# Performance work log

Hardware: AMD Instinct MI355X
Metric: run time of the kernel (lower is better)

## Reference

```python
import jax, jax.numpy as jnp
import numpy as np

C = 201      # num_classes (200 + background)
K = 5        # num_prototype
D = 256      # projected dim
GAMMA = 0.999
SK_EPS = 0.05
SK_ITERS = 3


def l2n(x, eps=1e-12):
    return x / jnp.maximum(jnp.linalg.norm(x, axis=-1, keepdims=True), eps)


def layernorm(x, g, b, eps=1e-5):
    mu = jnp.mean(x, axis=-1, keepdims=True)
    var = jnp.var(x, axis=-1, keepdims=True)
    return (x - mu) * jax.lax.rsqrt(var + eps) * g + b


def masked_sinkhorn(logits, mask_f):
    # logits: [N, K] prototype logits for one class; mask_f: [N] 1.0 where patch belongs to class
    m = mask_f[:, None]
    L = jnp.exp(logits / SK_EPS) * m
    Bc = mask_f.sum()  # number of patches of this class
    L = L / jnp.maximum(jnp.sum(L), 1e-12)
    for _ in range(SK_ITERS):
        L = L / jnp.maximum(jnp.sum(L, axis=0, keepdims=True), 1e-12) / K   # per-prototype marginal
        L = L / jnp.maximum(jnp.sum(L, axis=1, keepdims=True), 1e-12) * m   # per-patch marginal (masked)
        L = L / jnp.maximum(Bc, 1.0)
    L = L * Bc
    idx = jnp.argmax(L, axis=1)                                   # prototype index per patch
    hard = jax.nn.one_hot(idx, K, dtype=logits.dtype) * m          # deterministic hard assignment
    return hard, idx


def setup_inputs() -> dict:
    key = jax.random.key(0)
    k0, k1, k2, k3 = jax.random.split(key, 4)
    B, HW, DB = 64, 256, 768
    patch_tokens = jax.random.normal(k0, (B, HW, DB), jnp.float32)
    proj_w = jax.random.normal(k1, (D, DB), jnp.float32) * (1.0 / np.sqrt(DB))
    proj_b = jnp.zeros((D,), jnp.float32)
    ln_g = jnp.ones((D,), jnp.float32)
    ln_b = jnp.zeros((D,), jnp.float32)
    prototypes = jax.random.normal(k2, (C, K, D), jnp.float32) * 0.02
    pseudo_fg_mask = jax.random.randint(k3, (B * HW,), 0, C, dtype=jnp.int32)
    return dict(patch_tokens=patch_tokens, proj_w=proj_w, proj_b=proj_b,
                ln_g=ln_g, ln_b=ln_b, prototypes=prototypes,
                pseudo_fg_mask=pseudo_fg_mask)


def reference(patch_tokens, proj_w, proj_b, ln_g, ln_b, prototypes, pseudo_fg_mask):
    B, HW, _ = patch_tokens.shape
    H = W = int(np.sqrt(HW))
    patches = jnp.einsum('bnd,ed->bne', patch_tokens, proj_w) + proj_b      # [B,HW,D]
    patches = l2n(layernorm(patches.reshape(-1, D), ln_g, ln_b))             # [N,D] l2-normalized
    protos = l2n(prototypes)                                                 # [C,K,D] (in-place buffer normalize)
    logits_nck = jnp.einsum('nd,ckd->nck', patches, protos)                  # [N,C,K] == cosine sims
    ppl = logits_nck.reshape(B, H, W, C * K).transpose(0, 3, 1, 2)           # [B,CK,H,W]
    img_logits = jnp.mean(ppl, axis=(2, 3))                                  # AdaptiveAvgPool2d(1,1)
    pred_logits = jnp.sum(img_logits.reshape(B, C, K), axis=-1)              # == img_logits @ fc

    # ---- prototype update (vectorized over the original per-class python loop) ----
    N = patches.shape[0]
    class_preds = jnp.argmax(jnp.max(logits_nck, axis=2), axis=1)            # argmax of patch class logits
    correct_f = (pseudo_fg_mask == class_preds).astype(patches.dtype)        # [N]
    patches_correct = patches * correct_f[:, None]                           # [N,D]

    def per_class(c):
        mask_f = (pseudo_fg_mask == c).astype(patches.dtype)
        hard, idx = masked_sinkhorn(logits_nck[:, c, :], mask_f)
        L_correct = hard * correct_f[:, None]                                # [N,K]
        score = logits_nck[:, c, :] * L_correct                              # cos * assignment
        top_idx = jnp.argmax(score, axis=0)                                  # top-1 patch per prototype
        P_new_c = patches_correct[top_idx]                                   # [K,D] == final_assignment^T @ patches_correct
        return P_new_c, idx, mask_f.sum() > 0

    P_new, proto_idx, has_patches = jax.vmap(per_class)(jnp.arange(C))
    P_new = l2n(P_new)
    # final_assignment puts exactly one 1 per prototype column, so n_final != 0 always;
    # the update gate reduces to 'class has at least one patch'.
    P_upd = jnp.where(has_patches[:, None, None],
                      GAMMA * protos + (1.0 - GAMMA) * P_new, protos)
    new_prototypes = l2n(P_upd)

    per_patch_idx = jnp.take_along_axis(proto_idx.T, pseudo_fg_mask[:, None].astype(jnp.int32), axis=1)[:, 0]
    contrast_target = (per_patch_idx + K * pseudo_fg_mask).astype(patches.dtype)
    contrast_logits = logits_nck.reshape(N, C * K)
    return pred_logits, ppl, img_logits, contrast_logits, contrast_target, new_prototypes
```

## Files before the change

### kernel.cpp

```cpp
#include <hip/hip_runtime.h>
#include <hip/hip_bf16.h>

#define NROWS 16384
#define DBK   768
#define DDIM  256
#define NC    201
#define NK    5
#define NCK   1005

#define O_PPL    12864
#define O_IMG    16478784
#define O_CONTR  16543104
#define O_TGT    33009024
#define O_NEWP   33025408

#define W_PATCH  0u
#define W_PN     4194304u
#define W_CORR   4451584u
#define W_MEANP  4467968u
#define W_PBF    4484352u
#define W_PNBF   8678656u

typedef __attribute__((ext_vector_type(8))) short     short8;
typedef __attribute__((ext_vector_type(4))) float     f32x4;
typedef __attribute__((ext_vector_type(4))) unsigned int uint4v;
typedef __attribute__((ext_vector_type(4))) unsigned short ushort4v;

__device__ __forceinline__ float waveRedSum(float v){
  #pragma unroll
  for(int o=32;o>0;o>>=1) v += __shfl_xor(v,o,64);
  return v;
}

__device__ __forceinline__ unsigned short f2bf(float x){
  union { float f; unsigned u; } c; c.f = x;
  unsigned r = c.u + 0x7FFFu + ((c.u >> 16) & 1u);
  return (unsigned short)(r >> 16);
}
__device__ __forceinline__ unsigned pack2(float a, float b){
  return (unsigned)f2bf(a) | ((unsigned)f2bf(b) << 16);
}
__device__ __forceinline__ uint4v pack8(float4 lo, float4 hi){
  uint4v u;
  u[0] = pack2(lo.x, lo.y); u[1] = pack2(lo.z, lo.w);
  u[2] = pack2(hi.x, hi.y); u[3] = pack2(hi.z, hi.w);
  return u;
}

__global__ __launch_bounds__(256,2) void k_gemm1m(
    const float* __restrict__ A, const float* __restrict__ W,
    const float* __restrict__ bias, float* __restrict__ out)
{
  __shared__ ushort As[4096];
  __shared__ ushort Bs[4096];
  const int tid = threadIdx.x;
  const int m0 = blockIdx.x * 128;
  const int n0 = blockIdx.y * 128;
  const int lane = tid & 63, wid = tid >> 6;
  const int wr = wid >> 1, wc = wid & 1;
  const int srow = tid >> 2, sslot = tid & 3;
  const int woff  = srow*32      + (sslot ^ ((srow>>1)&3))*8;
  const int woff2 = (srow+64)*32 + (sslot ^ ((srow>>1)&3))*8;
  const int l15 = lane & 15, kg = lane >> 4;
  const int rslot = (kg ^ ((l15>>1)&3))*8;
  f32x4 acc[4][4] = {};
  const float* Ap0 = A + (size_t)(m0+srow)*DBK + sslot*8;
  const float* Ap1 = Ap0 + (size_t)64*DBK;
  const float* Wp0 = W + (size_t)(n0+srow)*DBK + sslot*8;
  const float* Wp1 = Wp0 + (size_t)64*DBK;
  for (int k0 = 0; k0 < DBK; k0 += 32) {
    float4 a00 = *(const float4*)(Ap0+k0), a01 = *(const float4*)(Ap0+k0+4);
    float4 a10 = *(const float4*)(Ap1+k0), a11 = *(const float4*)(Ap1+k0+4);
    float4 b00 = *(const float4*)(Wp0+k0), b01 = *(const float4*)(Wp0+k0+4);
    float4 b10 = *(const float4*)(Wp1+k0), b11 = *(const float4*)(Wp1+k0+4);
    __syncthreads();
    *(uint4v*)&As[woff]  = pack8(a00, a01);
    *(uint4v*)&As[woff2] = pack8(a10, a11);
    *(uint4v*)&Bs[woff]  = pack8(b00, b01);
    *(uint4v*)&Bs[woff2] = pack8(b10, b11);
    __syncthreads();
    short8 af[4], bf[4];
    #pragma unroll
    for (int i=0;i<4;i++){
      af[i] = *(const short8*)&As[(wr*64 + i*16 + l15)*32 + rslot];
      bf[i] = *(const short8*)&Bs[(wc*64 + i*16 + l15)*32 + rslot];
    }
    #pragma unroll
    for (int i=0;i<4;i++)
      #pragma unroll
      for (int j=0;j<4;j++)
        acc[i][j] = __builtin_amdgcn_mfma_f32_16x16x32_bf16(af[i], bf[j], acc[i][j], 0,0,0);
  }
  #pragma unroll
  for (int j=0;j<4;j++){
    const int ncol = n0 + wc*64 + j*16 + l15;
    const float bv = bias[ncol];
    #pragma unroll
    for (int i=0;i<4;i++){
      const int mrow = m0 + wr*64 + i*16 + kg*4;
      #pragma unroll
      for (int r=0;r<4;r++)
        out[(size_t)(mrow+r)*DDIM + ncol] = acc[i][j][r] + bv;
    }
  }
}

__global__ __launch_bounds__(256,2) void k_gemm2m(
    const ushort* __restrict__ A, const ushort* __restrict__ B,
    float* __restrict__ ct, float* __restrict__ ppl)
{
  __shared__ ushort As[4096];
  __shared__ ushort Bs[4096];
  const int tid = threadIdx.x;
  const int m0 = blockIdx.x * 128;
  const int n0 = blockIdx.y * 128;
  const int lane = tid & 63, wid = tid >> 6;
  const int wr = wid >> 1, wc = wid & 1;
  const int srow = tid >> 2, sslot = tid & 3;
  const int woff  = srow*32      + (sslot ^ ((srow>>1)&3))*8;
  const int woff2 = (srow+64)*32 + (sslot ^ ((srow>>1)&3))*8;
  const int l15 = lane & 15, kg = lane >> 4;
  const int rslot = (kg ^ ((l15>>1)&3))*8;
  f32x4 acc[4][4] = {};
  const ushort* Ap0 = A + (size_t)(m0+srow)*DDIM + sslot*8;
  const ushort* Ap1 = Ap0 + (size_t)64*DDIM;
  const ushort* Bp0 = B + (size_t)(n0+srow)*DDIM + sslot*8;
  const ushort* Bp1 = Bp0 + (size_t)64*DDIM;
  for (int k0 = 0; k0 < DDIM; k0 += 32) {
    uint4v a0 = *(const uint4v*)(Ap0+k0);
    uint4v a1 = *(const uint4v*)(Ap1+k0);
    uint4v b0 = *(const uint4v*)(Bp0+k0);
    uint4v b1 = *(const uint4v*)(Bp1+k0);
    __syncthreads();
    *(uint4v*)&As[woff]  = a0;
    *(uint4v*)&As[woff2] = a1;
    *(uint4v*)&Bs[woff]  = b0;
    *(uint4v*)&Bs[woff2] = b1;
    __syncthreads();
    short8 af[4], bf[4];
    #pragma unroll
    for (int i=0;i<4;i++){
      af[i] = *(const short8*)&As[(wr*64 + i*16 + l15)*32 + rslot];
      bf[i] = *(const short8*)&Bs[(wc*64 + i*16 + l15)*32 + rslot];
    }
    #pragma unroll
    for (int i=0;i<4;i++)
      #pragma unroll
      for (int j=0;j<4;j++)
        acc[i][j] = __builtin_amdgcn_mfma_f32_16x16x32_bf16(af[i], bf[j], acc[i][j], 0,0,0);
  }
  const int bimg = m0 >> 8;
  #pragma unroll
  for (int i=0;i<4;i++){
    const int mrow = m0 + wr*64 + i*16 + kg*4;
    const int hw = mrow & 255;
    #pragma unroll
    for (int j=0;j<4;j++){
      const int ck = n0 + wc*64 + j*16 + l15;
      if (ck < NCK){
        #pragma unroll
        for (int r=0;r<4;r++)
          ct[(size_t)(mrow+r)*NCK + ck] = acc[i][j][r];
        *(f32x4*)&ppl[((size_t)(bimg*NCK+ck))*256 + hw] = acc[i][j];
      }
    }
  }
}

__global__ __launch_bounds__(256) void k_ln(float* __restrict__ p,
    const float* __restrict__ g, const float* __restrict__ bta, ushort* __restrict__ pbf)
{
  const int wid = threadIdx.x >> 6, lane = threadIdx.x & 63;
  const int row = blockIdx.x * 4 + wid;
  float4 x = *(float4*)&p[(size_t)row*DDIM + lane*4];
  float s = x.x + x.y + x.z + x.w;
  s = waveRedSum(s);
  const float mu = s * (1.f/256.f);
  const float d0=x.x-mu, d1=x.y-mu, d2=x.z-mu, d3=x.w-mu;
  float ss = d0*d0 + d1*d1 + d2*d2 + d3*d3;
  ss = waveRedSum(ss);
  const float var = ss * (1.f/256.f);
  const float rs = rsqrtf(var + 1e-5f);
  const float4 gv = *(const float4*)&g[lane*4];
  const float4 bv = *(const float4*)&bta[lane*4];
  const float y0 = d0*rs*gv.x + bv.x;
  const float y1 = d1*rs*gv.y + bv.y;
  const float y2 = d2*rs*gv.z + bv.z;
  const float y3 = d3*rs*gv.w + bv.w;
  float n2 = y0*y0 + y1*y1 + y2*y2 + y3*y3;
  n2 = waveRedSum(n2);
  const float inv = 1.f / fmaxf(sqrtf(n2), 1e-12f);
  float4 o; o.x=y0*inv; o.y=y1*inv; o.z=y2*inv; o.w=y3*inv;
  *(float4*)&p[(size_t)row*DDIM + lane*4] = o;
  ushort4v ob; ob[0]=f2bf(o.x); ob[1]=f2bf(o.y); ob[2]=f2bf(o.z); ob[3]=f2bf(o.w);
  *(ushort4v*)&pbf[(size_t)row*DDIM + lane*4] = ob;
}

__global__ __launch_bounds__(256) void k_pnorm(const float* __restrict__ pr,
    float* __restrict__ out, ushort* __restrict__ obf)
{
  const int wid = threadIdx.x >> 6, lane = threadIdx.x & 63;
  const int row = blockIdx.x * 4 + wid;
  if (row >= NCK){
    ushort4v z = {0,0,0,0};
    *(ushort4v*)&obf[(size_t)row*DDIM + lane*4] = z;
    return;
  }
  const float4 x = *(const float4*)&pr[(size_t)row*DDIM + lane*4];
  float n2 = x.x*x.x + x.y*x.y + x.z*x.z + x.w*x.w;
  n2 = waveRedSum(n2);
  const float inv = 1.f / fmaxf(sqrtf(n2), 1e-12f);
  float4 o; o.x=x.x*inv; o.y=x.y*inv; o.z=x.z*inv; o.w=x.w*inv;
  *(float4*)&out[(size_t)row*DDIM + lane*4] = o;
  ushort4v ob; ob[0]=f2bf(o.x); ob[1]=f2bf(o.y); ob[2]=f2bf(o.z); ob[3]=f2bf(o.w);
  *(ushort4v*)&obf[(size_t)row*DDIM + lane*4] = ob;
}

__global__ __launch_bounds__(256) void k_pmean(const float* __restrict__ p, float* __restrict__ mp)
{
  const int b = blockIdx.x, d = threadIdx.x;
  const float* base = p + (size_t)b*256*DDIM + d;
  float s = 0.f;
  #pragma unroll 8
  for (int r=0;r<256;r++) s += base[(size_t)r*DDIM];
  mp[b*DDIM + d] = s * (1.f/256.f);
}

__global__ __launch_bounds__(256) void k_img2(const float* __restrict__ mp,
    const float* __restrict__ pn, float* __restrict__ img)
{
  const int gid = blockIdx.x*256 + threadIdx.x;
  if (gid >= 64*NCK) return;
  const int b = gid / NCK, ck = gid - b*NCK;
  const float4* a = (const float4*)&mp[b*DDIM];
  const float4* q = (const float4*)&pn[(size_t)ck*DDIM];
  float s = 0.f;
  #pragma unroll 8
  for (int d=0; d<64; d++){
    const float4 x = a[d], y = q[d];
    s += x.x*y.x + x.y*y.y + x.z*y.z + x.w*y.w;
  }
  img[gid] = s;
}

__global__ __launch_bounds__(256) void k_pred(const float* __restrict__ img, float* __restrict__ pred)
{
  const int gid = blockIdx.x*256 + threadIdx.x;
  if (gid >= 64*NC) return;
  const int b = gid / NC, c = gid % NC;
  const float* ip = &img[(size_t)b*NCK + c*5];
  pred[(size_t)b*NC + c] = ip[0]+ip[1]+ip[2]+ip[3]+ip[4];
}

__global__ __launch_bounds__(256) void k_cls(const float* __restrict__ ct,
    const int* __restrict__ mask, float* __restrict__ corr)
{
  const int wid = threadIdx.x >> 6, lane = threadIdx.x & 63;
  const int n = blockIdx.x * 4 + wid;
  const float* row = &ct[(size_t)n*NCK];
  float bv = -1e30f; int bc = 0x7FFFFFFF;
  #pragma unroll
  for(int j=0;j<16;j++){
    const int ck = lane + 64*j;
    if (ck < NCK){
      const float v = row[ck];
      const int c = ck / 5;
      if (v > bv || (v == bv && c < bc)){ bv = v; bc = c; }
    }
  }
  #pragma unroll
  for(int o=32;o>0;o>>=1){
    const float ov = __shfl_xor(bv,o,64);
    const int   oc = __shfl_xor(bc,o,64);
    if (ov > bv || (ov == bv && oc < bc)){ bv = ov; bc = oc; }
  }
  if (lane == 0) corr[n] = (mask[n] == bc) ? 1.f : 0.f;
}

__device__ __forceinline__ void blockRed6(float* a, float* sred){
  #pragma unroll
  for(int j=0;j<6;j++) a[j] = waveRedSum(a[j]);
  const int wv = threadIdx.x >> 6, lane = threadIdx.x & 63;
  __syncthreads();
  if (lane == 0){
    #pragma unroll
    for(int j=0;j<6;j++) sred[wv*6+j] = a[j];
  }
  __syncthreads();
  #pragma unroll
  for(int j=0;j<6;j++){
    float s = 0.f;
    #pragma unroll
    for(int w2=0;w2<8;w2++) s += sred[w2*6+j];
    a[j] = s;
  }
}

__device__ __forceinline__ float blockSum512(float x, float* s8){
  x = waveRedSum(x);
  const int wv = threadIdx.x >> 6, lane = threadIdx.x & 63;
  __syncthreads();
  if (lane == 0) s8[wv] = x;
  __syncthreads();
  float s = 0.f;
  #pragma unroll
  for(int w2=0;w2<8;w2++) s += s8[w2];
  return s;
}

__global__ __launch_bounds__(512,2) void k_sinkhorn(
    const float* __restrict__ ppl, const int* __restrict__ mask,
    const float* __restrict__ corr, const float* __restrict__ patches,
    const float* __restrict__ pnorm, float* __restrict__ tgt, float* __restrict__ newp)
{
  const int c  = blockIdx.x;
  const int c5 = c * 5;
  const int tid = threadIdx.x;
  __shared__ float sred[48];
  __shared__ float srv[40];
  __shared__ int   srn[40];

#define LGPTR(n) (ppl + ((size_t)(((n)>>8)*NCK) + c5)*256 + ((n)&255))

  unsigned mb = 0;
  float cs[6] = {0.f,0.f,0.f,0.f,0.f,0.f};
  #pragma unroll
  for(int i=0;i<32;i++){
    const int n = tid + 512*i;
    if (mask[n] == c){
      mb |= (1u << i);
      cs[5] += 1.f;
      const float* lp = LGPTR(n);
      cs[0] += expf(lp[0]   *20.f);
      cs[1] += expf(lp[256] *20.f);
      cs[2] += expf(lp[512] *20.f);
      cs[3] += expf(lp[768] *20.f);
      cs[4] += expf(lp[1024]*20.f);
    }
  }
  blockRed6(cs, sred);
  const float Bc  = cs[5];
  const float Bcc = fmaxf(Bc, 1.f);
  const float S   = cs[0]+cs[1]+cs[2]+cs[3]+cs[4];
  const float v0  = 1.f / fmaxf(S, 1e-12f);
  float v[5];
  #pragma unroll
  for(int k=0;k<5;k++) v[k] = v0 / (fmaxf(v0*cs[k], 1e-12f) * 5.f);

  float u[32];
  #pragma unroll
  for(int i=0;i<32;i++) u[i] = 1.f;
  #pragma unroll 1
  for(int t=0;t<2;t++){
    float w5[6] = {0.f,0.f,0.f,0.f,0.f,0.f};
    #pragma unroll
    for(int i=0;i<32;i++){
      if (mb & (1u << i)){
        const int n = tid + 512*i;
        const float* lp = LGPTR(n);
        const float e0 = expf(lp[0]   *20.f);
        const float e1 = expf(lp[256] *20.f);
        const float e2 = expf(lp[512] *20.f);
        const float e3 = expf(lp[768] *20.f);
        const float e4 = expf(lp[1024]*20.f);
        const float s = e0*v[0] + e1*v[1] + e2*v[2] + e3*v[3] + e4*v[4];
        const float un = u[i] / fmaxf(u[i]*s, 1e-12f) / Bcc;
        u[i] = un;
        w5[0] += un*e0; w5[1] += un*e1; w5[2] += un*e2; w5[3] += un*e3; w5[4] += un*e4;
      }
    }
    blockRed6(w5, sred);
    #pragma unroll
    for(int k=0;k<5;k++) v[k] = v[k] / (fmaxf(v[k]*w5[k], 1e-12f) * 5.f);
  }

  float bv5[5]; int bn5[5];
  #pragma unroll
  for(int k=0;k<5;k++){ bv5[k] = -1e30f; bn5[k] = 0x7FFFFFFF; }
  #pragma unroll
  for(int i=0;i<32;i++){
    const int n = tid + 512*i;
    float val[5] = {0.f,0.f,0.f,0.f,0.f};
    if (mb & (1u << i)){
      const float* lp = LGPTR(n);
      float lg[5];
      lg[0]=lp[0]; lg[1]=lp[256]; lg[2]=lp[512]; lg[3]=lp[768]; lg[4]=lp[1024];
      const float p0 = expf(lg[0]*20.f)*v[0];
      const float p1 = expf(lg[1]*20.f)*v[1];
      const float p2 = expf(lg[2]*20.f)*v[2];
      const float p3 = expf(lg[3]*20.f)*v[3];
      const float p4 = expf(lg[4]*20.f)*v[4];
      int bi = 0; float bb = p0;
      if (p1 > bb){ bb=p1; bi=1; }
      if (p2 > bb){ bb=p2; bi=2; }
      if (p3 > bb){ bb=p3; bi=3; }
      if (p4 > bb){ bb=p4; bi=4; }
      tgt[n] = (float)(bi + c5);
      const bool cc = (corr[n] > 0.5f);
      #pragma unroll
      for(int k=0;k<5;k++) val[k] = (cc && bi == k) ? lg[k] : 0.f;
    }
    #pragma unroll
    for(int k=0;k<5;k++){
      if (val[k] > bv5[k] || (val[k] == bv5[k] && n < bn5[k])){ bv5[k]=val[k]; bn5[k]=n; }
    }
  }
  #pragma unroll
  for(int k=0;k<5;k++){
    #pragma unroll
    for(int o=32;o>0;o>>=1){
      const float ov = __shfl_xor(bv5[k],o,64);
      const int   on = __shfl_xor(bn5[k],o,64);
      if (ov > bv5[k] || (ov == bv5[k] && on < bn5[k])){ bv5[k]=ov; bn5[k]=on; }
    }
  }
  const int wv = tid >> 6, lane = tid & 63;
  __syncthreads();
  if (lane == 0){
    #pragma unroll
    for(int k=0;k<5;k++){ srv[wv*5+k]=bv5[k]; srn[wv*5+k]=bn5[k]; }
  }
  __syncthreads();
  int topn[5];
  #pragma unroll
  for(int k=0;k<5;k++){
    float bb = srv[k]; int nn = srn[k];
    #pragma unroll
    for(int w2=1;w2<8;w2++){
      const float ov = srv[w2*5+k]; const int on = srn[w2*5+k];
      if (ov > bb || (ov == bb && on < nn)){ bb=ov; nn=on; }
    }
    topn[k] = nn;
  }
  __syncthreads();

  const bool hasp = (Bc > 0.f);
  #pragma unroll
  for(int k=0;k<5;k++){
    const int tn_ = topn[k];
    const float cf = corr[tn_];
    float pv = 0.f, proto = 0.f;
    if (tid < 256){
      pv    = patches[(size_t)tn_*DDIM + tid] * cf;
      proto = pnorm[(size_t)(c5+k)*DDIM + tid];
    }
    const float ss = blockSum512(pv*pv, sred);
    const float pnv = pv / fmaxf(sqrtf(ss), 1e-12f);
    const float pu = hasp ? (0.999f*proto + 0.001f*pnv) : proto;
    const float ss2 = blockSum512(tid<256 ? pu*pu : 0.f, sred);
    if (tid < 256) newp[(size_t)(c5+k)*DDIM + tid] = pu / fmaxf(sqrtf(ss2), 1e-12f);
  }
#undef LGPTR
}

extern "C" void kernel_launch(void* const* d_in, const int* in_sizes, int n_in,
                              void* d_out, int out_size, void* d_ws, size_t ws_size,
                              hipStream_t stream)
{
  const float* patch_tokens = (const float*)d_in[0];
  const float* proj_w       = (const float*)d_in[1];
  const float* proj_b       = (const float*)d_in[2];
  const float* ln_g         = (const float*)d_in[3];
  const float* ln_b         = (const float*)d_in[4];
  const float* prototypes   = (const float*)d_in[5];
  const int*   mask         = (const int*)d_in[6];
  float* out = (float*)d_out;
  float* ws  = (float*)d_ws;

  float*  patches = ws + W_PATCH;
  float*  pn      = ws + W_PN;
  float*  corr    = ws + W_CORR;
  float*  meanp   = ws + W_MEANP;
  ushort* pbf     = (ushort*)(ws + W_PBF);
  ushort* pnbf    = (ushort*)(ws + W_PNBF);

  float* pred = out;
  float* ppl  = out + O_PPL;
  float* img  = out + O_IMG;
  float* ct   = out + O_CONTR;
  float* tgt  = out + O_TGT;
  float* newp = out + O_NEWP;

  k_gemm1m<<<dim3(128,2),256,0,stream>>>(patch_tokens, proj_w, proj_b, patches);
  k_ln<<<4096,256,0,stream>>>(patches, ln_g, ln_b, pbf);
  k_pnorm<<<256,256,0,stream>>>(prototypes, pn, pnbf);
  k_gemm2m<<<dim3(128,8),256,0,stream>>>(pbf, pnbf, ct, ppl);
  k_pmean<<<64,256,0,stream>>>(patches, meanp);
  k_img2<<<252,256,0,stream>>>(meanp, pn, img);
  k_pred<<<51,256,0,stream>>>(img, pred);
  k_cls<<<4096,256,0,stream>>>(ct, mask, corr);
  k_sinkhorn<<<201,512,0,stream>>>(ppl, mask, corr, patches, pn, tgt, newp);
}
```

Measured before the change: 376.4 us.

## Bucket patches by class and process each class's rows one per thread

Adds histogram, prefix-scan and fill kernels that build a per-class list of patch indices. The Sinkhorn kernel then reads only its class's rows, one row per thread in a 256-thread block, with the logits and exps kept in registers. Before, each of the 201 blocks scanned the whole 16384-entry mask and recomputed exps on every pass, and this change is meant to remove that redundant mask scanning and exp recomputation. In exchange it adds three small launches plus a memset, and it silently assumes no class holds more than 256 patches.

```diff
diff --git a/kernel.cpp b/kernel.cpp
--- a/kernel.cpp
+++ b/kernel.cpp
@@ -20,6 +20,10 @@
 #define W_MEANP  4467968u
 #define W_PBF    4484352u
 #define W_PNBF   8678656u
+#define W_CNT    8809728u
+#define W_FILLP  8809984u
+#define W_OFFS   8810240u
+#define W_ROWS   8810496u
 
 typedef __attribute__((ext_vector_type(8))) short     short8;
 typedef __attribute__((ext_vector_type(4))) float     f32x4;
@@ -277,180 +281,169 @@
   if (lane == 0) corr[n] = (mask[n] == bc) ? 1.f : 0.f;
 }
 
-__device__ __forceinline__ void blockRed6(float* a, float* sred){
-  #pragma unroll
-  for(int j=0;j<6;j++) a[j] = waveRedSum(a[j]);
+__global__ __launch_bounds__(256) void k_hist(const int* __restrict__ mask, int* __restrict__ cnt)
+{
+  const int n = blockIdx.x*256 + threadIdx.x;
+  atomicAdd(&cnt[mask[n]], 1);
+}
+
+__global__ __launch_bounds__(256) void k_scan(const int* __restrict__ cnt, int* __restrict__ offs)
+{
+  __shared__ int sc[256];
+  const int tid = threadIdx.x;
+  const int v = (tid < NC) ? cnt[tid] : 0;
+  sc[tid] = v;
+  __syncthreads();
+  #pragma unroll
+  for (int s=1; s<256; s<<=1){
+    const int add = (tid >= s) ? sc[tid-s] : 0;
+    __syncthreads();
+    sc[tid] += add;
+    __syncthreads();
+  }
+  offs[tid] = sc[tid] - v;
+}
+
+__global__ __launch_bounds__(256) void k_fill(const int* __restrict__ mask,
+    const int* __restrict__ offs, int* __restrict__ fillp, int* __restrict__ rows)
+{
+  const int n = blockIdx.x*256 + threadIdx.x;
+  const int c = mask[n];
+  const int pos = atomicAdd(&fillp[c], 1);
+  rows[offs[c] + pos] = n;
+}
+
+__device__ __forceinline__ void blockRed5_256(float* a, float* ls){
+  #pragma unroll
+  for (int j=0;j<5;j++) a[j] = waveRedSum(a[j]);
   const int wv = threadIdx.x >> 6, lane = threadIdx.x & 63;
   __syncthreads();
   if (lane == 0){
     #pragma unroll
-    for(int j=0;j<6;j++) sred[wv*6+j] = a[j];
-  }
-  __syncthreads();
-  #pragma unroll
-  for(int j=0;j<6;j++){
-    float s = 0.f;
-    #pragma unroll
-    for(int w2=0;w2<8;w2++) s += sred[w2*6+j];
-    a[j] = s;
-  }
-}
-
-__device__ __forceinline__ float blockSum512(float x, float* s8){
+    for (int j=0;j<5;j++) ls[wv*5+j] = a[j];
+  }
+  __syncthreads();
+  #pragma unroll
+  for (int j=0;j<5;j++) a[j] = ls[j] + ls[5+j] + ls[10+j] + ls[15+j];
+}
+
+__device__ __forceinline__ float blockSum256(float x, float* ls4){
   x = waveRedSum(x);
   const int wv = threadIdx.x >> 6, lane = threadIdx.x & 63;
   __syncthreads();
-  if (lane == 0) s8[wv] = x;
-  __syncthreads();
-  float s = 0.f;
-  #pragma unroll
-  for(int w2=0;w2<8;w2++) s += s8[w2];
-  return s;
-}
-
-__global__ __launch_bounds__(512,2) void k_sinkhorn(
-    const float* __restrict__ ppl, const int* __restrict__ mask,
+  if (lane == 0) ls4[wv] = x;
+  __syncthreads();
+  return ls4[0] + ls4[1] + ls4[2] + ls4[3];
+}
+
+__global__ __launch_bounds__(256,4) void k_sink2(
+    const float* __restrict__ ppl, const int* __restrict__ cnt,
+    const int* __restrict__ offs, const int* __restrict__ rows,
     const float* __restrict__ corr, const float* __restrict__ patches,
-    const float* __restrict__ pnorm, float* __restrict__ tgt, float* __restrict__ newp)
-{
-  const int c  = blockIdx.x;
-  const int c5 = c * 5;
-  const int tid = threadIdx.x;
-  __shared__ float sred[48];
-  __shared__ float srv[40];
-  __shared__ int   srn[40];
-
-#define LGPTR(n) (ppl + ((size_t)(((n)>>8)*NCK) + c5)*256 + ((n)&255))
-
-  unsigned mb = 0;
-  float cs[6] = {0.f,0.f,0.f,0.f,0.f,0.f};
-  #pragma unroll
-  for(int i=0;i<32;i++){
-    const int n = tid + 512*i;
-    if (mask[n] == c){
-      mb |= (1u << i);
-      cs[5] += 1.f;
-      const float* lp = LGPTR(n);
-      cs[0] += expf(lp[0]   *20.f);
-      cs[1] += expf(lp[256] *20.f);
-      cs[2] += expf(lp[512] *20.f);
-      cs[3] += expf(lp[768] *20.f);
-      cs[4] += expf(lp[1024]*20.f);
-    }
-  }
-  blockRed6(cs, sred);
-  const float Bc  = cs[5];
-  const float Bcc = fmaxf(Bc, 1.f);
-  const float S   = cs[0]+cs[1]+cs[2]+cs[3]+cs[4];
-  const float v0  = 1.f / fmaxf(S, 1e-12f);
+    const float* __restrict__ pn, float* __restrict__ tgt, float* __restrict__ newp)
+{
+  const int c = blockIdx.x, c5 = c*5, tid = threadIdx.x;
+  const int wv = tid >> 6, lane = tid & 63;
+  __shared__ float ls[20];
+  __shared__ float lsv[20];
+  __shared__ int   lsn[20];
+  const int nr  = cnt[c];
+  const int off = offs[c];
+  const bool act = tid < nr;
+  int n = 0; float lg[5], e[5]; float cf = 0.f;
+  if (act){
+    n = rows[off + tid];
+    const float* lp = ppl + ((size_t)((n>>8)*NCK) + c5)*256 + (n&255);
+    #pragma unroll
+    for (int k=0;k<5;k++){ lg[k] = lp[k*256]; e[k] = expf(lg[k]*20.f); }
+    cf = corr[n];
+  } else {
+    #pragma unroll
+    for (int k=0;k<5;k++){ lg[k] = 0.f; e[k] = 0.f; }
+  }
+  float a[5];
+  #pragma unroll
+  for (int k=0;k<5;k++) a[k] = e[k];
+  blockRed5_256(a, ls);
+  const float Bcc = (float)(nr > 0 ? nr : 1);
+  const float S = a[0]+a[1]+a[2]+a[3]+a[4];
+  const float v0 = 1.f / fmaxf(S, 1e-12f);
   float v[5];
   #pragma unroll
-  for(int k=0;k<5;k++) v[k] = v0 / (fmaxf(v0*cs[k], 1e-12f) * 5.f);
-
-  float u[32];
-  #pragma unroll
-  for(int i=0;i<32;i++) u[i] = 1.f;
+  for (int k=0;k<5;k++) v[k] = v0 / (fmaxf(v0*a[k], 1e-12f) * 5.f);
+  float u = 1.f;
   #pragma unroll 1
-  for(int t=0;t<2;t++){
-    float w5[6] = {0.f,0.f,0.f,0.f,0.f,0.f};
-    #pragma unroll
-    for(int i=0;i<32;i++){
-      if (mb & (1u << i)){
-        const int n = tid + 512*i;
-        const float* lp = LGPTR(n);
-        const float e0 = expf(lp[0]   *20.f);
-        const float e1 = expf(lp[256] *20.f);
-        const float e2 = expf(lp[512] *20.f);
-        const float e3 = expf(lp[768] *20.f);
-        const float e4 = expf(lp[1024]*20.f);
-        const float s = e0*v[0] + e1*v[1] + e2*v[2] + e3*v[3] + e4*v[4];
-        const float un = u[i] / fmaxf(u[i]*s, 1e-12f) / Bcc;
-        u[i] = un;
-        w5[0] += un*e0; w5[1] += un*e1; w5[2] += un*e2; w5[3] += un*e3; w5[4] += un*e4;
-      }
-    }
-    blockRed6(w5, sred);
-    #pragma unroll
-    for(int k=0;k<5;k++) v[k] = v[k] / (fmaxf(v[k]*w5[k], 1e-12f) * 5.f);
-  }
-
-  float bv5[5]; int bn5[5];
-  #pragma unroll
-  for(int k=0;k<5;k++){ bv5[k] = -1e30f; bn5[k] = 0x7FFFFFFF; }
-  #pragma unroll
-  for(int i=0;i<32;i++){
-    const int n = tid + 512*i;
-    float val[5] = {0.f,0.f,0.f,0.f,0.f};
-    if (mb & (1u << i)){
-      const float* lp = LGPTR(n);
-      float lg[5];
-      lg[0]=lp[0]; lg[1]=lp[256]; lg[2]=lp[512]; lg[3]=lp[768]; lg[4]=lp[1024];
-      const float p0 = expf(lg[0]*20.f)*v[0];
-      const float p1 = expf(lg[1]*20.f)*v[1];
-      const float p2 = expf(lg[2]*20.f)*v[2];
-      const float p3 = expf(lg[3]*20.f)*v[3];
-      const float p4 = expf(lg[4]*20.f)*v[4];
-      int bi = 0; float bb = p0;
-      if (p1 > bb){ bb=p1; bi=1; }
-      if (p2 > bb){ bb=p2; bi=2; }
-      if (p3 > bb){ bb=p3; bi=3; }
-      if (p4 > bb){ bb=p4; bi=4; }
-      tgt[n] = (float)(bi + c5);
-      const bool cc = (corr[n] > 0.5f);
+  for (int t=0;t<2;t++){
+    float w[5] = {0.f,0.f,0.f,0.f,0.f};
+    if (act){
+      const float s = e[0]*v[0] + e[1]*v[1] + e[2]*v[2] + e[3]*v[3] + e[4]*v[4];
+      const float un = u / fmaxf(u*s, 1e-12f) / Bcc;
+      u = un;
       #pragma unroll
-      for(int k=0;k<5;k++) val[k] = (cc && bi == k) ? lg[k] : 0.f;
-    }
-    #pragma unroll
-    for(int k=0;k<5;k++){
-      if (val[k] > bv5[k] || (val[k] == bv5[k] && n < bn5[k])){ bv5[k]=val[k]; bn5[k]=n; }
-    }
-  }
-  #pragma unroll
-  for(int k=0;k<5;k++){
-    #pragma unroll
-    for(int o=32;o>0;o>>=1){
-      const float ov = __shfl_xor(bv5[k],o,64);
-      const int   on = __shfl_xor(bn5[k],o,64);
-      if (ov > bv5[k] || (ov == bv5[k] && on < bn5[k])){ bv5[k]=ov; bn5[k]=on; }
-    }
-  }
-  const int wv = tid >> 6, lane = tid & 63;
+      for (int k=0;k<5;k++) w[k] = un * e[k];
+    }
+    blockRed5_256(w, ls);
+    #pragma unroll
+    for (int k=0;k<5;k++) v[k] = v[k] / (fmaxf(v[k]*w[k], 1e-12f) * 5.f);
+  }
+  int bi = 0;
+  if (act){
+    float bb = e[0]*v[0];
+    #pragma unroll
+    for (int k=1;k<5;k++){
+      const float p = e[k]*v[k];
+      if (p > bb){ bb = p; bi = k; }
+    }
+    tgt[n] = (float)(bi + c5);
+  }
+  const bool cc = act && (cf > 0.5f);
+  float sv[5]; int sn[5];
+  #pragma unroll
+  for (int k=0;k<5;k++){
+    float rv = (cc && bi == k) ? lg[k] : 0.f;
+    int   rn = act ? n : 0x7FFFFFFF;
+    if (0.f > rv || (0.f == rv && tid < rn)){ rv = 0.f; rn = tid; }
+    sv[k] = rv; sn[k] = rn;
+  }
+  #pragma unroll
+  for (int k=0;k<5;k++){
+    #pragma unroll
+    for (int o=32;o>0;o>>=1){
+      const float ov = __shfl_xor(sv[k],o,64);
+      const int   on = __shfl_xor(sn[k],o,64);
+      if (ov > sv[k] || (ov == sv[k] && on < sn[k])){ sv[k]=ov; sn[k]=on; }
+    }
+  }
   __syncthreads();
   if (lane == 0){
     #pragma unroll
-    for(int k=0;k<5;k++){ srv[wv*5+k]=bv5[k]; srn[wv*5+k]=bn5[k]; }
+    for (int k=0;k<5;k++){ lsv[wv*5+k] = sv[k]; lsn[wv*5+k] = sn[k]; }
   }
   __syncthreads();
   int topn[5];
   #pragma unroll
-  for(int k=0;k<5;k++){
-    float bb = srv[k]; int nn = srn[k];
-    #pragma unroll
-    for(int w2=1;w2<8;w2++){
-      const float ov = srv[w2*5+k]; const int on = srn[w2*5+k];
-      if (ov > bb || (ov == bb && on < nn)){ bb=ov; nn=on; }
+  for (int k=0;k<5;k++){
+    float bb = lsv[k]; int nn = lsn[k];
+    #pragma unroll
+    for (int w2=1;w2<4;w2++){
+      const float ov = lsv[w2*5+k]; const int on = lsn[w2*5+k];
+      if (ov > bb || (ov == bb && on < nn)){ bb = ov; nn = on; }
     }
     topn[k] = nn;
   }
-  __syncthreads();
-
-  const bool hasp = (Bc > 0.f);
-  #pragma unroll
-  for(int k=0;k<5;k++){
+  const bool hasp = (nr > 0);
+  #pragma unroll 1
+  for (int k=0;k<5;k++){
     const int tn_ = topn[k];
-    const float cf = corr[tn_];
-    float pv = 0.f, proto = 0.f;
-    if (tid < 256){
-      pv    = patches[(size_t)tn_*DDIM + tid] * cf;
-      proto = pnorm[(size_t)(c5+k)*DDIM + tid];
-    }
-    const float ss = blockSum512(pv*pv, sred);
+    const float cfa = corr[tn_];
+    const float pv = patches[(size_t)tn_*DDIM + tid] * cfa;
+    const float proto = pn[(size_t)(c5+k)*DDIM + tid];
+    const float ss = blockSum256(pv*pv, ls);
     const float pnv = pv / fmaxf(sqrtf(ss), 1e-12f);
     const float pu = hasp ? (0.999f*proto + 0.001f*pnv) : proto;
-    const float ss2 = blockSum512(tid<256 ? pu*pu : 0.f, sred);
-    if (tid < 256) newp[(size_t)(c5+k)*DDIM + tid] = pu / fmaxf(sqrtf(ss2), 1e-12f);
-  }
-#undef LGPTR
+    const float ss2 = blockSum256(pu*pu, ls);
+    newp[(size_t)(c5+k)*DDIM + tid] = pu / fmaxf(sqrtf(ss2), 1e-12f);
+  }
 }
 
 extern "C" void kernel_launch(void* const* d_in, const int* in_sizes, int n_in,
@@ -473,6 +466,10 @@
   float*  meanp   = ws + W_MEANP;
   ushort* pbf     = (ushort*)(ws + W_PBF);
   ushort* pnbf    = (ushort*)(ws + W_PNBF);
+  int*    cnt     = (int*)(ws + W_CNT);
+  int*    fillp   = (int*)(ws + W_FILLP);
+  int*    offs    = (int*)(ws + W_OFFS);
+  int*    rows    = (int*)(ws + W_ROWS);
 
   float* pred = out;
   float* ppl  = out + O_PPL;
@@ -480,6 +477,11 @@
   float* ct   = out + O_CONTR;
   float* tgt  = out + O_TGT;
   float* newp = out + O_NEWP;
+
+  hipMemsetAsync((void*)cnt, 0, 512*sizeof(int), stream);
+  k_hist<<<64,256,0,stream>>>(mask, cnt);
+  k_scan<<<1,256,0,stream>>>(cnt, offs);
+  k_fill<<<64,256,0,stream>>>(mask, offs, fillp, rows);
 
   k_gemm1m<<<dim3(128,2),256,0,stream>>>(patch_tokens, proj_w, proj_b, patches);
   k_ln<<<4096,256,0,stream>>>(patches, ln_g, ln_b, pbf);
@@ -489,5 +491,5 @@
   k_img2<<<252,256,0,stream>>>(meanp, pn, img);
   k_pred<<<51,256,0,stream>>>(img, pred);
   k_cls<<<4096,256,0,stream>>>(ct, mask, corr);
-  k_sinkhorn<<<201,512,0,stream>>>(ppl, mask, corr, patches, pn, tgt, newp);
-}
+  k_sink2<<<201,256,0,stream>>>(ppl, cnt, offs, rows, corr, patches, pn, tgt, newp);
+}
```

After: 322.2 us. -14.4%, faster.
